# Kernel optimization log

Hardware: AMD Instinct MI355X
Metric: run time of the kernel (lower is better)

Reference implementation:

```python
import jax, jax.numpy as jnp
import numpy as np

N = 50000          # num nodes (adj_dim)
D = 128            # feature dim
E = 1_600_000      # num edges
C = 1.0            # curvature c_in
NUM_GCN_LAYERS = 3 # num_layers - 1
MIN_NORM = 1e-15
EPS = 1e-5


def hyp_logmap0(x, c):
    # Hyperboloid (Lorentz) logmap at origin, per HGCF manifold code.
    sqrtK = 1.0 / jnp.sqrt(c)            # sqrt(K), K = 1/c
    y = x[..., 1:]                        # spatial part [N, D-1]
    y_norm = jnp.maximum(jnp.linalg.norm(y, axis=-1, keepdims=True), MIN_NORM)
    theta = jnp.maximum(x[..., 0:1] / sqrtK, 1.0 + EPS)
    tail = sqrtK * jnp.arccosh(theta) * y / y_norm
    return jnp.concatenate([jnp.zeros_like(x[..., 0:1]), tail], axis=-1)


def hyp_expmap0(u, c):
    sqrtK = 1.0 / jnp.sqrt(c)
    v = u[..., 1:]
    v_norm = jnp.maximum(jnp.linalg.norm(v, axis=-1, keepdims=True), MIN_NORM)
    theta = v_norm / sqrtK
    first = sqrtK * jnp.cosh(theta)
    tail = sqrtK * jnp.sinh(theta) * v / v_norm
    return jnp.concatenate([first, tail], axis=-1)


def hyp_proj(x, c):
    # Project onto hyperboloid: reset time-like coord from spatial norm.
    K = 1.0 / c
    y = x[..., 1:]
    y_sqnorm = jnp.sum(y * y, axis=-1, keepdims=True)
    first = jnp.sqrt(jnp.maximum(K + y_sqnorm, EPS))
    return jnp.concatenate([first, y], axis=-1)


def spmm(rows, cols, vals, h):
    # sparse [N,N] @ dense [N,D] via gather + segment_sum
    return jax.ops.segment_sum(vals[:, None] * h[cols], rows, num_segments=N)


def setup_inputs() -> dict:
    key = jax.random.key(0)
    k1, k2, k3, k4 = jax.random.split(key, 4)
    # Build valid hyperboloid points: tangent vector at origin (time coord 0),
    # then expmap0 + proj.
    u_tail = 0.1 * jax.random.normal(k1, (N, D - 1), dtype=jnp.float32)
    u = jnp.concatenate([jnp.zeros((N, 1), jnp.float32), u_tail], axis=-1)
    x = hyp_proj(hyp_expmap0(u, C), C)
    adj_rows = jax.random.randint(k2, (E,), 0, N, dtype=jnp.int32)
    adj_cols = jax.random.randint(k3, (E,), 0, N, dtype=jnp.int32)
    # roughly degree-normalized positive edge weights
    adj_vals = jax.random.uniform(k4, (E,), dtype=jnp.float32) / 32.0
    return {"x": x, "adj_rows": adj_rows, "adj_cols": adj_cols, "adj_vals": adj_vals}


def reference(x, adj_rows, adj_cols, adj_vals):
    # HypAgg.forward with network='plainGCN'
    h = hyp_logmap0(x, C)
    for _ in range(NUM_GCN_LAYERS):
        h = spmm(adj_rows, adj_cols, adj_vals, h)
    out = hyp_proj(hyp_expmap0(h, C), C)
    # HyperbolicGraphConvolution returns (h, adj); adj passes through unchanged,
    # so the tensor output is `out`.
    return out
```

## Files before the change

### kernel.cpp

```cpp
#include <hip/hip_runtime.h>
#include <hip/hip_fp16.h>
#include <math.h>

#define N_NODES 50000
#define D 128
#define MIN_NORM 1e-15f
#define EPS 1e-5f
#define NBUCK 196
#define CHUNK 4096
#define CAP 12288
#define FSCALE 32.0f
#define INV_FSCALE (1.0f / 32.0f)

typedef float fx2 __attribute__((ext_vector_type(2)));

__global__ __launch_bounds__(256) void binA_kernel(const int* __restrict__ rows,
                                                   const int* __restrict__ cols,
                                                   const float* __restrict__ vals,
                                                   int* __restrict__ gcur,
                                                   int2* __restrict__ tmp, int E) {
    __shared__ int lh[NBUCK];
    __shared__ int lb[NBUCK];
    for (int i = threadIdx.x; i < NBUCK; i += 256) lh[i] = 0;
    __syncthreads();
    int start = blockIdx.x * CHUNK;
    int end = min(start + CHUNK, E);
    for (int i = start + threadIdx.x; i < end; i += 256)
        atomicAdd(&lh[rows[i] >> 8], 1);
    __syncthreads();
    for (int i = threadIdx.x; i < NBUCK; i += 256) {
        int c = lh[i];
        lb[i] = i * CAP + (c ? atomicAdd(&gcur[i], c) : 0);
        lh[i] = 0;
    }
    __syncthreads();
    for (int i = start + threadIdx.x; i < end; i += 256) {
        int r = rows[i];
        int b = r >> 8;
        int ofs = atomicAdd(&lh[b], 1);
        tmp[lb[b] + ofs] = make_int2(((r & 255) << 16) | cols[i], __float_as_int(vals[i]));
    }
}

__global__ __launch_bounds__(256) void binB_kernel(const int2* __restrict__ tmp,
                                                   const int* __restrict__ gcur,
                                                   int2* __restrict__ rowptr2,
                                                   unsigned* __restrict__ epay) {
    __shared__ int hist[256];
    __shared__ int wsum[4];
    int b = blockIdx.x;
    int base = b * CAP;
    int nloc = gcur[b];
    hist[threadIdx.x] = 0;
    __syncthreads();
    for (int i = threadIdx.x; i < nloc; i += 256)
        atomicAdd(&hist[tmp[base + i].x >> 16], 1);
    __syncthreads();
    int lane = threadIdx.x & 63, wid = threadIdx.x >> 6;
    int v = hist[threadIdx.x];
    int x = v;
    #pragma unroll
    for (int off = 1; off < 64; off <<= 1) {
        int t = __shfl_up(x, off, 64);
        if (lane >= off) x += t;
    }
    if (lane == 63) wsum[wid] = x;
    __syncthreads();
    if (threadIdx.x == 0) {
        int s0 = wsum[0], s1 = wsum[1], s2 = wsum[2];
        wsum[0] = 0; wsum[1] = s0; wsum[2] = s0 + s1; wsum[3] = s0 + s1 + s2;
    }
    __syncthreads();
    int excl = x - v + wsum[wid];
    int g = (b << 8) + threadIdx.x;
    if (g < N_NODES) rowptr2[g] = make_int2(base + excl, base + excl + v);
    __syncthreads();
    hist[threadIdx.x] = excl;
    __syncthreads();
    for (int i = threadIdx.x; i < nloc; i += 256) {
        int2 p = tmp[base + i];
        int rl = p.x >> 16;
        unsigned col = (unsigned)(p.x & 0xffff);
        unsigned vb = (unsigned)__half_as_ushort(__float2half(__int_as_float(p.y)));
        int pos = base + atomicAdd(&hist[rl], 1);
        epay[pos] = (col << 16) | vb;
    }
}

__global__ void logmap0_kernel(const float* __restrict__ x, unsigned short* __restrict__ h) {
    int row = blockIdx.x;
    int lane = threadIdx.x;
    const float2* xr = reinterpret_cast<const float2*>(x + (size_t)row * D);
    float2 v = xr[lane];
    float x0 = __shfl(v.x, 0, 64);
    float sq = v.y * v.y + (lane == 0 ? 0.0f : v.x * v.x);
    #pragma unroll
    for (int off = 1; off < 64; off <<= 1) sq += __shfl_xor(sq, off, 64);
    float ynorm = fmaxf(sqrtf(sq), MIN_NORM);
    float theta = fmaxf(x0, 1.0f + EPS);
    float scale = FSCALE * acoshf(theta) / ynorm;
    float ox = (lane == 0) ? 0.0f : v.x * scale;
    float oy = v.y * scale;
    int packed = __builtin_amdgcn_cvt_pk_fp8_f32(ox, oy, 0, false);
    h[(size_t)row * (D / 2) + lane] = (unsigned short)packed;
}

template <bool FINAL>
__global__ __launch_bounds__(256) void spmm_kernel(const int2* __restrict__ rowptr2,
                                                   const unsigned* __restrict__ epay,
                                                   const unsigned short* __restrict__ hin,
                                                   void* __restrict__ hout) {
    int wid = threadIdx.x >> 6, lane = threadIdx.x & 63;
    int row = blockIdx.x * 4 + wid;
    if (row >= N_NODES) return;
    int2 rp = rowptr2[row];
    int j = rp.x, end = rp.y;
    int n = end - j;
    int half = lane >> 5;
    int l32 = lane & 31;
    unsigned laneoff = (unsigned)(l32 << 2);
    const char* hb = (const char*)hin;
    const unsigned* ep = epay + j + half;
    float a0 = 0.f, a1 = 0.f, a2 = 0.f, a3 = 0.f;
    int iters = n >> 1;
    #pragma unroll 4
    for (int t = 0; t < iters; ++t) {
        unsigned P = ep[2 * t];
        unsigned off = ((P & 0xffff0000u) >> 9) + laneoff;
        unsigned g = *(const unsigned*)(hb + off);
        fx2 flo = __builtin_amdgcn_cvt_pk_f32_fp8((int)g, false);
        fx2 fhi = __builtin_amdgcn_cvt_pk_f32_fp8((int)g, true);
        float vv = __half2float(__ushort_as_half((unsigned short)(P & 0xffffu)));
        a0 = fmaf(vv, flo.x, a0); a1 = fmaf(vv, flo.y, a1);
        a2 = fmaf(vv, fhi.x, a2); a3 = fmaf(vv, fhi.y, a3);
    }
    if (n & 1) {
        unsigned P = epay[end - 1];
        unsigned off = ((P & 0xffff0000u) >> 9) + laneoff;
        unsigned g = *(const unsigned*)(hb + off);
        fx2 flo = __builtin_amdgcn_cvt_pk_f32_fp8((int)g, false);
        fx2 fhi = __builtin_amdgcn_cvt_pk_f32_fp8((int)g, true);
        float vv = half ? 0.0f
                        : __half2float(__ushort_as_half((unsigned short)(P & 0xffffu)));
        a0 = fmaf(vv, flo.x, a0); a1 = fmaf(vv, flo.y, a1);
        a2 = fmaf(vv, fhi.x, a2); a3 = fmaf(vv, fhi.y, a3);
    }
    a0 += __shfl_xor(a0, 32, 64);
    a1 += __shfl_xor(a1, 32, 64);
    a2 += __shfl_xor(a2, 32, 64);
    a3 += __shfl_xor(a3, 32, 64);
    if (!FINAL) {
        int pk0 = __builtin_amdgcn_cvt_pk_fp8_f32(a0, a1, 0, false);
        int pk1 = __builtin_amdgcn_cvt_pk_fp8_f32(a2, a3, 0, false);
        if (half == 0)
            ((unsigned*)hout)[(size_t)row * 32 + l32] =
                ((unsigned)pk0 & 0xffffu) | ((unsigned)pk1 << 16);
    } else {
        a0 *= INV_FSCALE; a1 *= INV_FSCALE; a2 *= INV_FSCALE; a3 *= INV_FSCALE;
        float sq = a1 * a1 + a2 * a2 + a3 * a3 + (l32 == 0 ? 0.0f : a0 * a0);
        #pragma unroll
        for (int off = 1; off < 32; off <<= 1) sq += __shfl_xor(sq, off, 64);
        float vn = fmaxf(sqrtf(sq), MIN_NORM);
        float sh = sinhf(vn);
        float scale = sh / vn;
        float first = sqrtf(fmaxf(1.0f + sh * sh, EPS));
        float4 o;
        o.x = (l32 == 0) ? first : a0 * scale;
        o.y = a1 * scale;
        o.z = a2 * scale;
        o.w = a3 * scale;
        if (half == 0)
            reinterpret_cast<float4*>((float*)hout + (size_t)row * D)[l32] = o;
    }
}

extern "C" void kernel_launch(void* const* d_in, const int* in_sizes, int n_in,
                              void* d_out, int out_size, void* d_ws, size_t ws_size,
                              hipStream_t stream) {
    const float* x    = (const float*)d_in[0];
    const int*   rows = (const int*)d_in[1];
    const int*   cols = (const int*)d_in[2];
    const float* vals = (const float*)d_in[3];
    float* out = (float*)d_out;
    int E = in_sizes[1];

    char* ws = (char*)d_ws;
    int2*           tmp  = (int2*)ws;
    unsigned short* hA   = (unsigned short*)ws;
    unsigned short* hB   = (unsigned short*)(ws + (size_t)N_NODES * D);
    unsigned* epay    = (unsigned*)(ws + (size_t)NBUCK * CAP * 8);
    int2*     rowptr2 = (int2*)(epay + (size_t)NBUCK * CAP);
    int*      gcur    = (int*)(rowptr2 + N_NODES);

    int eb = (E + CHUNK - 1) / CHUNK;
    int sb = (N_NODES + 3) / 4;

    hipMemsetAsync(gcur, 0, NBUCK * sizeof(int), stream);
    binA_kernel<<<eb, 256, 0, stream>>>(rows, cols, vals, gcur, tmp, E);
    binB_kernel<<<NBUCK, 256, 0, stream>>>(tmp, gcur, rowptr2, epay);

    logmap0_kernel<<<N_NODES, 64, 0, stream>>>(x, hA);

    spmm_kernel<false><<<sb, 256, 0, stream>>>(rowptr2, epay, hA, hB);
    spmm_kernel<false><<<sb, 256, 0, stream>>>(rowptr2, epay, hB, hA);
    spmm_kernel<true ><<<sb, 256, 0, stream>>>(rowptr2, epay, hA, out);
}
```

Baseline: 186.6 us.

## Use full-wave per-row SpMM with 8-byte fp32 edge payloads and 8-way unroll

Edge payloads become uint2 holding a pre-shifted byte offset (col<<7) and the fp32 weight, replacing the packed 16-bit column plus fp16 weight. The SpMM now has each lane handle two features over all edges of the row, instead of splitting edges across two half-waves that are then combined by a shuffle. The edge loop is unrolled 8-way with two accumulator pairs, and row bounds are made wave-uniform via readfirstlane. CAP is reduced to shrink the bucket regions. The intent is fewer decode ops and more loads in flight per wave, paid for with doubled edge-payload bandwidth and narrower 2-byte gathers per lane.

```diff
diff --git a/kernel.cpp b/kernel.cpp
--- a/kernel.cpp
+++ b/kernel.cpp
@@ -1,5 +1,4 @@
 #include <hip/hip_runtime.h>
-#include <hip/hip_fp16.h>
 #include <math.h>
 
 #define N_NODES 50000
@@ -8,7 +7,7 @@
 #define EPS 1e-5f
 #define NBUCK 196
 #define CHUNK 4096
-#define CAP 12288
+#define CAP 9216
 #define FSCALE 32.0f
 #define INV_FSCALE (1.0f / 32.0f)
 
@@ -45,7 +44,7 @@
 __global__ __launch_bounds__(256) void binB_kernel(const int2* __restrict__ tmp,
                                                    const int* __restrict__ gcur,
                                                    int2* __restrict__ rowptr2,
-                                                   unsigned* __restrict__ epay) {
+                                                   uint2* __restrict__ epay) {
     __shared__ int hist[256];
     __shared__ int wsum[4];
     int b = blockIdx.x;
@@ -81,9 +80,8 @@
         int2 p = tmp[base + i];
         int rl = p.x >> 16;
         unsigned col = (unsigned)(p.x & 0xffff);
-        unsigned vb = (unsigned)__half_as_ushort(__float2half(__int_as_float(p.y)));
         int pos = base + atomicAdd(&hist[rl], 1);
-        epay[pos] = (col << 16) | vb;
+        epay[pos] = make_uint2(col << 7, (unsigned)p.y);
     }
 }
 
@@ -107,70 +105,48 @@
 
 template <bool FINAL>
 __global__ __launch_bounds__(256) void spmm_kernel(const int2* __restrict__ rowptr2,
-                                                   const unsigned* __restrict__ epay,
+                                                   const uint2* __restrict__ epay,
                                                    const unsigned short* __restrict__ hin,
                                                    void* __restrict__ hout) {
-    int wid = threadIdx.x >> 6, lane = threadIdx.x & 63;
-    int row = blockIdx.x * 4 + wid;
-    if (row >= N_NODES) return;
+    int lane = threadIdx.x & 63;
+    int row = __builtin_amdgcn_readfirstlane(blockIdx.x * 4 + (threadIdx.x >> 6));
     int2 rp = rowptr2[row];
-    int j = rp.x, end = rp.y;
-    int n = end - j;
-    int half = lane >> 5;
-    int l32 = lane & 31;
-    unsigned laneoff = (unsigned)(l32 << 2);
+    int j   = __builtin_amdgcn_readfirstlane(rp.x);
+    int end = __builtin_amdgcn_readfirstlane(rp.y);
     const char* hb = (const char*)hin;
-    const unsigned* ep = epay + j + half;
-    float a0 = 0.f, a1 = 0.f, a2 = 0.f, a3 = 0.f;
-    int iters = n >> 1;
-    #pragma unroll 4
-    for (int t = 0; t < iters; ++t) {
-        unsigned P = ep[2 * t];
-        unsigned off = ((P & 0xffff0000u) >> 9) + laneoff;
-        unsigned g = *(const unsigned*)(hb + off);
-        fx2 flo = __builtin_amdgcn_cvt_pk_f32_fp8((int)g, false);
-        fx2 fhi = __builtin_amdgcn_cvt_pk_f32_fp8((int)g, true);
-        float vv = __half2float(__ushort_as_half((unsigned short)(P & 0xffffu)));
-        a0 = fmaf(vv, flo.x, a0); a1 = fmaf(vv, flo.y, a1);
-        a2 = fmaf(vv, fhi.x, a2); a3 = fmaf(vv, fhi.y, a3);
+    int lo = lane << 1;
+    float a0 = 0.f, a1 = 0.f, b0 = 0.f, b1 = 0.f;
+#define EDGE(E, A0, A1) {                                                     \
+    unsigned short g8 = *(const unsigned short*)(hb + (E).x + lo);            \
+    fx2 f = __builtin_amdgcn_cvt_pk_f32_fp8((int)g8, false);                  \
+    float vv = __uint_as_float((E).y);                                        \
+    A0 = fmaf(vv, f.x, A0); A1 = fmaf(vv, f.y, A1); }
+    int t = j;
+    for (; t + 8 <= end; t += 8) {
+        uint2 e0 = epay[t],     e1 = epay[t + 1], e2 = epay[t + 2], e3 = epay[t + 3];
+        uint2 e4 = epay[t + 4], e5 = epay[t + 5], e6 = epay[t + 6], e7 = epay[t + 7];
+        EDGE(e0, a0, a1); EDGE(e1, b0, b1); EDGE(e2, a0, a1); EDGE(e3, b0, b1);
+        EDGE(e4, a0, a1); EDGE(e5, b0, b1); EDGE(e6, a0, a1); EDGE(e7, b0, b1);
     }
-    if (n & 1) {
-        unsigned P = epay[end - 1];
-        unsigned off = ((P & 0xffff0000u) >> 9) + laneoff;
-        unsigned g = *(const unsigned*)(hb + off);
-        fx2 flo = __builtin_amdgcn_cvt_pk_f32_fp8((int)g, false);
-        fx2 fhi = __builtin_amdgcn_cvt_pk_f32_fp8((int)g, true);
-        float vv = half ? 0.0f
-                        : __half2float(__ushort_as_half((unsigned short)(P & 0xffffu)));
-        a0 = fmaf(vv, flo.x, a0); a1 = fmaf(vv, flo.y, a1);
-        a2 = fmaf(vv, fhi.x, a2); a3 = fmaf(vv, fhi.y, a3);
-    }
-    a0 += __shfl_xor(a0, 32, 64);
-    a1 += __shfl_xor(a1, 32, 64);
-    a2 += __shfl_xor(a2, 32, 64);
-    a3 += __shfl_xor(a3, 32, 64);
+    for (; t < end; ++t) { uint2 e = epay[t]; EDGE(e, a0, a1); }
+#undef EDGE
+    a0 += b0; a1 += b1;
     if (!FINAL) {
-        int pk0 = __builtin_amdgcn_cvt_pk_fp8_f32(a0, a1, 0, false);
-        int pk1 = __builtin_amdgcn_cvt_pk_fp8_f32(a2, a3, 0, false);
-        if (half == 0)
-            ((unsigned*)hout)[(size_t)row * 32 + l32] =
-                ((unsigned)pk0 & 0xffffu) | ((unsigned)pk1 << 16);
+        int pk = __builtin_amdgcn_cvt_pk_fp8_f32(a0, a1, 0, false);
+        ((unsigned short*)hout)[(size_t)row * (D / 2) + lane] = (unsigned short)pk;
     } else {
-        a0 *= INV_FSCALE; a1 *= INV_FSCALE; a2 *= INV_FSCALE; a3 *= INV_FSCALE;
-        float sq = a1 * a1 + a2 * a2 + a3 * a3 + (l32 == 0 ? 0.0f : a0 * a0);
+        a0 *= INV_FSCALE; a1 *= INV_FSCALE;
+        float sq = a1 * a1 + (lane == 0 ? 0.0f : a0 * a0);
         #pragma unroll
-        for (int off = 1; off < 32; off <<= 1) sq += __shfl_xor(sq, off, 64);
+        for (int off = 1; off < 64; off <<= 1) sq += __shfl_xor(sq, off, 64);
         float vn = fmaxf(sqrtf(sq), MIN_NORM);
         float sh = sinhf(vn);
         float scale = sh / vn;
         float first = sqrtf(fmaxf(1.0f + sh * sh, EPS));
-        float4 o;
-        o.x = (l32 == 0) ? first : a0 * scale;
+        float2 o;
+        o.x = (lane == 0) ? first : a0 * scale;
         o.y = a1 * scale;
-        o.z = a2 * scale;
-        o.w = a3 * scale;
-        if (half == 0)
-            reinterpret_cast<float4*>((float*)hout + (size_t)row * D)[l32] = o;
+        reinterpret_cast<float2*>((float*)hout + (size_t)row * D)[lane] = o;
     }
 }
 
@@ -185,11 +161,12 @@
     int E = in_sizes[1];
 
     char* ws = (char*)d_ws;
+    size_t REG = (size_t)NBUCK * CAP;
     int2*           tmp  = (int2*)ws;
     unsigned short* hA   = (unsigned short*)ws;
     unsigned short* hB   = (unsigned short*)(ws + (size_t)N_NODES * D);
-    unsigned* epay    = (unsigned*)(ws + (size_t)NBUCK * CAP * 8);
-    int2*     rowptr2 = (int2*)(epay + (size_t)NBUCK * CAP);
+    uint2*    epay    = (uint2*)(ws + REG * 8);
+    int2*     rowptr2 = (int2*)(ws + REG * 16);
     int*      gcur    = (int*)(rowptr2 + N_NODES);
 
     int eb = (E + CHUNK - 1) / CHUNK;
```

Measured after the change: 181.7 us. 2.6% less time.
